# Kernel optimization log

Hardware: AMD Instinct MI355X
Metric: run time of the kernel (lower is better)

Reference implementation:

```python
import jax, jax.numpy as jnp
import numpy as np

NEG = -9e15
LN_EPS = 1e-5
ALPHA = 0.2  # LeakyReLU negative slope


def setup_inputs() -> dict:
    key = jax.random.key(0)
    ks = jax.random.split(key, 10)
    B, N, Din, H, F, L = 8, 512, 64, 8, 128, 2
    x = jax.random.normal(ks[0], (B, N, Din), dtype=jnp.float32)
    adj = jax.random.randint(ks[1], (B, N, N), 0, 2, dtype=jnp.int32)
    Wp = jax.random.normal(ks[2], (Din, F), dtype=jnp.float32) * 0.12
    bp = jnp.zeros((F,), dtype=jnp.float32)
    W_heads = jax.random.normal(ks[3], (L, H, F, F), dtype=jnp.float32) * 0.08
    a_heads = jax.random.normal(ks[4], (L, H, 2 * F), dtype=jnp.float32) * 0.08
    W_out = jax.random.normal(ks[5], (L, H * F, F), dtype=jnp.float32) * 0.03
    a_out = jax.random.normal(ks[6], (L, 2 * F), dtype=jnp.float32) * 0.08
    ln_g = jnp.ones((L, F), dtype=jnp.float32)
    ln_b = jnp.zeros((L, F), dtype=jnp.float32)
    return {"x": x, "adj": adj, "Wp": Wp, "bp": bp, "W_heads": W_heads,
            "a_heads": a_heads, "W_out": W_out, "a_out": a_out,
            "ln_g": ln_g, "ln_b": ln_b}


def _gat_heads(x, W, a, adj_mask):
    # x:[B,N,Fin]  W:[H,Fin,F]  a:[H,2F]  adj_mask:[B,N,N] bool
    h = jnp.einsum('bni,hio->bhno', x, W)          # [B,H,N,F]
    F = h.shape[-1]
    # a_input @ a == (h_i . a1) + (h_j . a2): split attention vector,
    # mathematically identical to the concat formulation.
    s1 = jnp.einsum('bhnf,hf->bhn', h, a[:, :F])   # source term
    s2 = jnp.einsum('bhnf,hf->bhn', h, a[:, F:])   # target term
    e = jax.nn.leaky_relu(s1[:, :, :, None] + s2[:, :, None, :], ALPHA)  # [B,H,N,N]
    att = jnp.where(adj_mask[:, None], e, NEG)
    att = jax.nn.softmax(att, axis=-1)
    return jnp.einsum('bhnm,bhmf->bhnf', att, h)   # [B,H,N,F]


def _gat_single(x, W, a, adj_mask):
    # out_att head (concat=False, no ELU)
    h = jnp.einsum('bni,io->bno', x, W)            # [B,N,F]
    F = h.shape[-1]
    s1 = h @ a[:F]                                  # [B,N]
    s2 = h @ a[F:]
    e = jax.nn.leaky_relu(s1[:, :, None] + s2[:, None, :], ALPHA)
    att = jnp.where(adj_mask, e, NEG)
    att = jax.nn.softmax(att, axis=-1)
    return jnp.einsum('bnm,bmf->bnf', att, h)


def _layernorm(x, g, b):
    mu = jnp.mean(x, axis=-1, keepdims=True)
    var = jnp.var(x, axis=-1, keepdims=True)
    return (x - mu) * jax.lax.rsqrt(var + LN_EPS) * g + b


def reference(x, adj, Wp, bp, W_heads, a_heads, W_out, a_out, ln_g, ln_b):
    adj_mask = adj > 0                              # [B,N,N]
    L = W_heads.shape[0]
    B, N = x.shape[0], x.shape[1]
    # input projection (eval mode -> dropout is identity)
    h = jax.nn.relu(x @ Wp + bp)                    # [B,N,F]
    for i in range(L):
        residual = h
        heads = _gat_heads(h, W_heads[i], a_heads[i], adj_mask)      # [B,H,N,F]
        heads = jax.nn.elu(heads)                                     # concat=True -> ELU
        multi = jnp.transpose(heads, (0, 2, 1, 3)).reshape(B, N, -1)  # [B,N,H*F]
        out = _gat_single(multi, W_out[i], a_out[i], adj_mask)        # [B,N,F]
        h = _layernorm(out + residual, ln_g[i], ln_b[i])
        if i < L - 1:
            h = jax.nn.relu(h)
    return h
```

## Files before the change

### kernel.cpp

```cpp
#include <hip/hip_runtime.h>


constexpr int B = 8, N = 512, DIN = 64, H = 8, F = 128;
constexpr int BN = B * N;
constexpr float ALPHA_LR = 0.2f;
constexpr float EPS_LN = 1e-5f;
constexpr float FLOW = -3.0e38f;

typedef __attribute__((ext_vector_type(8))) short short8;
typedef __attribute__((ext_vector_type(4))) float f32x4;

__device__ __forceinline__ f32x4 mfma16(short8 a, short8 b, f32x4 c) {
  return __builtin_amdgcn_mfma_f32_16x16x32_bf16(a, b, c, 0, 0, 0);
}

__device__ __forceinline__ short f2bf(float f) {
  union { float f; unsigned u; } v;
  v.f = f;
  unsigned r = v.u + 0x7FFFu + ((v.u >> 16) & 1u);
  return (short)(r >> 16);
}

__global__ __launch_bounds__(256) void g_setup(
    const float* __restrict__ x, const int* __restrict__ adj,
    const float* __restrict__ Wp, const float* __restrict__ bp,
    const float* __restrict__ W_heads, const float* __restrict__ W_out,
    float* __restrict__ h, short* __restrict__ hb,
    unsigned long long* __restrict__ amask, short* __restrict__ WTh,
    short* __restrict__ WoT, float* __restrict__ sA) {
  __shared__ float T[32][33];
  __shared__ float xr[2][64];
  int bid = blockIdx.x, tid = threadIdx.x;
  for (int i = tid; i < 288; i += 256) sA[(size_t)bid * 288 + i] = 0.f;
  {
    int lane = tid & 63, wv = tid >> 6;
    int v[16];
#pragma unroll
    for (int j = 0; j < 16; j++) {
      int w = (bid + j * 512) * 4 + wv;
      v[j] = adj[(size_t)w * 64 + lane];
    }
#pragma unroll
    for (int j = 0; j < 16; j++) {
      int w = (bid + j * 512) * 4 + wv;
      unsigned long long m = __ballot(v[j] > 0);
      if (lane == 0) amask[w] = m;
    }
  }
  {
    int half = tid >> 7, f = tid & 127;
    int b = bid & 7, v0 = bid >> 3;
    for (int v = v0; v < 256; v += 64) {
      int row = b * 512 + v * 2 + half;
      __syncthreads();
      if (f < 64) xr[half][f] = x[(size_t)row * DIN + f];
      __syncthreads();
      float acc = bp[f];
#pragma unroll
      for (int i = 0; i < DIN; i++)
        acc = fmaf(xr[half][i], Wp[i * F + f], acc);
      acc = fmaxf(acc, 0.f);
      h[(size_t)row * F + f] = acc;
      hb[(size_t)row * F + f] = f2bf(acc);
    }
  }
  {
    const float* in; short* out; int R, C, bx, by, bt;
    if (bid < 256) {
      in = W_heads; out = WTh; R = 128; C = 128;
      bx = bid & 3; by = (bid >> 2) & 3; bt = bid >> 4;
    } else {
      int i = bid - 256;
      in = W_out; out = WoT; R = 1024; C = 128;
      bx = i & 3; by = (i >> 2) & 31; bt = i >> 7;
    }
    int c0 = bx * 32, r0 = by * 32;
    const float* ip = in + (size_t)bt * R * C;
    short* op = out + (size_t)bt * R * C;
    __syncthreads();
    {
      int r = tid >> 3, c4 = (tid & 7) * 4;
      float4 v = *(const float4*)(ip + (size_t)(r0 + r) * C + c0 + c4);
      T[r][c4] = v.x; T[r][c4 + 1] = v.y; T[r][c4 + 2] = v.z; T[r][c4 + 3] = v.w;
    }
    __syncthreads();
    {
      int cr = tid >> 3, q = (tid & 7) * 4;
      short4 o;
      o.x = f2bf(T[q][cr]); o.y = f2bf(T[q + 1][cr]);
      o.z = f2bf(T[q + 2][cr]); o.w = f2bf(T[q + 3][cr]);
      *(short4*)(op + (size_t)(c0 + cr) * R + r0 + q) = o;
    }
  }
}

__global__ __launch_bounds__(256) void k_proj_heads_mfma2(
    const short* __restrict__ WT, const short* __restrict__ hb,
    const float* __restrict__ ah_base, short* __restrict__ hhT,
    float* __restrict__ s1, float* __restrict__ s2) {
  int bid = blockIdx.x;
  int b = bid & 7, hd = (bid >> 3) & 7, ft = (bid >> 6) & 1, nt = bid >> 7;
  int bh = b * 8 + hd;
  int n0 = nt * 64;
  constexpr int LK = 136;
  __shared__ short As[64 * LK];
  __shared__ short Bs[64 * LK];
  int tid = threadIdx.x, lane = tid & 63, w = tid >> 6;
  {
    int r = tid >> 2, q = tid & 3;
    const uint4* g = (const uint4*)(WT + ((size_t)hd * F + ft * 64 + r) * F) + q * 4;
    uint4* lp = (uint4*)(As + r * LK) + q * 4;
    lp[0] = g[0]; lp[1] = g[1]; lp[2] = g[2]; lp[3] = g[3];
  }
  {
    int r = tid >> 2, q = tid & 3;
    const uint4* g = (const uint4*)(hb + ((size_t)(b * N + n0 + r)) * F) + q * 4;
    uint4* lp = (uint4*)(Bs + r * LK) + q * 4;
    lp[0] = g[0]; lp[1] = g[1]; lp[2] = g[2]; lp[3] = g[3];
  }
  __syncthreads();
  int arow = lane & 15, koff = (lane >> 4) * 8;
  f32x4 acc[4] = {};
#pragma unroll
  for (int ks = 0; ks < 4; ks++) {
    short8 bb = *(const short8*)(Bs + (w * 16 + arow) * LK + ks * 32 + koff);
#pragma unroll
    for (int rt = 0; rt < 4; rt++) {
      short8 a = *(const short8*)(As + (rt * 16 + arow) * LK + ks * 32 + koff);
      acc[rt] = mfma16(a, bb, acc[rt]);
    }
  }
  short* outp = hhT + (size_t)bh * F * N;
  int crow0 = (lane >> 4) * 4;
#pragma unroll
  for (int rt = 0; rt < 4; rt++) {
    int fo = ft * 64 + rt * 16 + crow0;
    int n = n0 + w * 16 + arow;
#pragma unroll
    for (int r = 0; r < 4; r++)
      outp[(size_t)(fo + r) * N + n] = f2bf(acc[rt][r]);
  }
  const float* ah = ah_base + (size_t)hd * 2 * F;
  float pa1 = 0.f, pa2 = 0.f;
#pragma unroll
  for (int rt = 0; rt < 4; rt++) {
    int fo = ft * 64 + rt * 16 + crow0;
#pragma unroll
    for (int r = 0; r < 4; r++) {
      pa1 = fmaf(ah[fo + r], acc[rt][r], pa1);
      pa2 = fmaf(ah[F + fo + r], acc[rt][r], pa2);
    }
  }
  pa1 += __shfl_xor(pa1, 16); pa1 += __shfl_xor(pa1, 32);
  pa2 += __shfl_xor(pa2, 16); pa2 += __shfl_xor(pa2, 32);
  if (lane < 16) {
    int n = n0 + w * 16 + lane;
    atomicAdd(&s1[(size_t)bh * N + n], pa1);
    atomicAdd(&s2[(size_t)bh * N + n], pa2);
  }
}

__global__ __launch_bounds__(256) void k_attn_heads4(
    const short* __restrict__ VT, const float* __restrict__ s1g,
    const float* __restrict__ s2g, const unsigned long long* __restrict__ amask,
    short* __restrict__ multi) {
  int bid = blockIdx.x;
  int b = bid & 7, hd = (bid >> 3) & 7, nt = bid >> 6;
  int bh = b * 8 + hd;
  int n0 = nt * 32;
  constexpr int LVK = 72;
  __shared__ short Vs[128 * LVK];
  __shared__ short Pf[4 * 64 * 8];
  __shared__ float s2all[512];
  __shared__ float s1r[32], mrow[32], linv[32];
  __shared__ float red[32][8];

  int tid = threadIdx.x, lane = tid & 63, w = tid >> 6;
  s2all[tid] = s2g[(size_t)bh * N + tid];
  s2all[tid + 256] = s2g[(size_t)bh * N + tid + 256];
  if (tid < 32) s1r[tid] = s1g[(size_t)bh * N + n0 + tid];
  __syncthreads();
  {
    int r = tid & 31, seg = tid >> 5;
    unsigned long long mb = amask[((size_t)(b * N + n0 + r)) * 8 + seg];
    unsigned lo = (unsigned)mb, hi = (unsigned)(mb >> 32);
    int base = seg * 64;
    float mx = FLOW;
#pragma unroll
    for (int k = 0; k < 32; k++) {
      mx = ((lo >> k) & 1u) ? fmaxf(mx, s2all[base + k]) : mx;
      mx = ((hi >> k) & 1u) ? fmaxf(mx, s2all[base + 32 + k]) : mx;
    }
    red[r][seg] = mx;
  }
  __syncthreads();
  if (tid < 32) {
    float m2 = FLOW;
#pragma unroll
    for (int k = 0; k < 8; k++) m2 = fmaxf(m2, red[tid][k]);
    float xm = s1r[tid] + m2;
    mrow[tid] = xm > 0.f ? xm : ALPHA_LR * xm;
  }
  int prow = ((w >> 1) << 4) | (lane & 15);
  int pcol = ((w & 1) << 5) + ((lane >> 4) << 3);
  int pg = ((w & 1) << 2) | (lane >> 4);
  const unsigned long long* mp = amask + ((size_t)(b * N + n0 + prow)) * 8;
  float lp = 0.f;
  int arow = lane & 15, koff = (lane >> 4) * 8;
  f32x4 acc[2][2] = {};
  const short* Vg = VT + (size_t)bh * F * N;
  int fr = tid >> 1, hf = tid & 1;
  for (int mc = 0; mc < 8; mc++) {
    int m0 = mc * 64;
    __syncthreads();
    {
      const uint4* g4 = (const uint4*)(Vg + (size_t)fr * N + m0 + hf * 32);
      uint4* l4 = (uint4*)(Vs + fr * LVK + hf * 32);
      l4[0] = g4[0]; l4[1] = g4[1]; l4[2] = g4[2]; l4[3] = g4[3];
    }
    {
      float s1v = s1r[prow], mr = mrow[prow];
      unsigned bits = (unsigned)((mp[mc] >> pcol) & 0xffull);
      short8 pk;
#pragma unroll
      for (int j = 0; j < 8; j++) {
        float xv = s1v + s2all[m0 + pcol + j];
        xv = xv > 0.f ? xv : ALPHA_LR * xv;
        float p = __expf(xv - mr);
        p = ((bits >> j) & 1u) ? p : 0.f;
        lp += p;
        pk[j] = f2bf(p);
      }
      *(short8*)(Pf + (w * 64 + lane) * 8) = pk;
    }
    __syncthreads();
#pragma unroll
    for (int ks = 0; ks < 2; ks++) {
      short8 a0 = *(const short8*)(Pf + ((0 * 2 + ks) * 64 + lane) * 8);
      short8 a1 = *(const short8*)(Pf + ((1 * 2 + ks) * 64 + lane) * 8);
#pragma unroll
      for (int cj = 0; cj < 2; cj++) {
        short8 bb = *(const short8*)(Vs + ((w * 2 + cj) * 16 + arow) * LVK +
                                     ks * 32 + koff);
        acc[0][cj] = mfma16(a0, bb, acc[0][cj]);
        acc[1][cj] = mfma16(a1, bb, acc[1][cj]);
      }
    }
  }
  __syncthreads();
  red[prow][pg] = lp;
  __syncthreads();
  if (tid < 32) {
    float ls = 0.f;
#pragma unroll
    for (int k = 0; k < 8; k++) ls += red[tid][k];
    linv[tid] = 1.f / ls;
  }
  __syncthreads();
  int crow0 = (lane >> 4) * 4;
#pragma unroll
  for (int rt = 0; rt < 2; rt++)
#pragma unroll
    for (int cj = 0; cj < 2; cj++) {
      int fcol = (w * 2 + cj) * 16 + arow;
#pragma unroll
      for (int rr = 0; rr < 4; rr++) {
        int nrow = rt * 16 + crow0 + rr;
        float v = acc[rt][cj][rr] * linv[nrow];
        v = v > 0.f ? v : __expf(v) - 1.f;
        multi[((size_t)(b * N + n0 + nrow)) * (H * F) + hd * F + fcol] = f2bf(v);
      }
    }
}

__global__ __launch_bounds__(256) void k_proj_out_mfma(
    const short* __restrict__ WoT, const short* __restrict__ multi,
    const float* __restrict__ ao, short* __restrict__ hsT,
    float* __restrict__ s1, float* __restrict__ s2) {
  int bid = blockIdx.x;
  int b = bid & 7, ft = (bid >> 3) & 3, nt = bid >> 5;
  constexpr int LK = 136;
  __shared__ short As[32 * LK];
  __shared__ short Bs[64 * LK];
  int tid = threadIdx.x, lane = tid & 63, w = tid >> 6;
  int arow = lane & 15, koff = (lane >> 4) * 8;
  const int KT = H * F;
  f32x4 acc[2] = {};
  for (int k0 = 0; k0 < KT; k0 += 128) {
    __syncthreads();
    {
      int r = tid >> 3, e = tid & 7;
      const uint4* gp = (const uint4*)(WoT + (size_t)(ft * 32 + r) * KT + k0) + e * 2;
      uint4* lp = (uint4*)(As + r * LK) + e * 2;
      lp[0] = gp[0]; lp[1] = gp[1];
    }
    {
      int r = tid >> 2, q = tid & 3;
      const uint4* gp =
          (const uint4*)(multi + (size_t)(b * N + nt * 64 + r) * KT + k0) + q * 4;
      uint4* lp = (uint4*)(Bs + r * LK) + q * 4;
      lp[0] = gp[0]; lp[1] = gp[1]; lp[2] = gp[2]; lp[3] = gp[3];
    }
    __syncthreads();
#pragma unroll
    for (int ks = 0; ks < 4; ks++) {
      short8 b0 = *(const short8*)(Bs + (w * 16 + arow) * LK + ks * 32 + koff);
      short8 a0 = *(const short8*)(As + arow * LK + ks * 32 + koff);
      short8 a1 = *(const short8*)(As + (16 + arow) * LK + ks * 32 + koff);
      acc[0] = mfma16(a0, b0, acc[0]);
      acc[1] = mfma16(a1, b0, acc[1]);
    }
  }
  int crow0 = (lane >> 4) * 4;
  short* op = hsT + (size_t)b * F * N;
#pragma unroll
  for (int rt = 0; rt < 2; rt++)
#pragma unroll
    for (int r = 0; r < 4; r++)
      op[(size_t)(ft * 32 + rt * 16 + crow0 + r) * N + nt * 64 + w * 16 + arow] =
          f2bf(acc[rt][r]);
  float pa1 = 0.f, pa2 = 0.f;
#pragma unroll
  for (int rt = 0; rt < 2; rt++) {
    int fo = ft * 32 + rt * 16 + crow0;
#pragma unroll
    for (int r = 0; r < 4; r++) {
      pa1 = fmaf(ao[fo + r], acc[rt][r], pa1);
      pa2 = fmaf(ao[F + fo + r], acc[rt][r], pa2);
    }
  }
  pa1 += __shfl_xor(pa1, 16); pa1 += __shfl_xor(pa1, 32);
  pa2 += __shfl_xor(pa2, 16); pa2 += __shfl_xor(pa2, 32);
  if (lane < 16) {
    int n = nt * 64 + w * 16 + lane;
    atomicAdd(&s1[(size_t)b * N + n], pa1);
    atomicAdd(&s2[(size_t)b * N + n], pa2);
  }
}

template <int LAST>
__global__ __launch_bounds__(256) void k_attn_single3(
    const short* __restrict__ VT, const float* __restrict__ s1g,
    const float* __restrict__ s2g, const unsigned long long* __restrict__ amask,
    const float* __restrict__ resid, const float* __restrict__ lng,
    const float* __restrict__ lnb, float* __restrict__ hout,
    short* __restrict__ hbout, float* __restrict__ dout) {
  int bid = blockIdx.x;
  int b = bid & 7, nt = bid >> 3;
  int n0 = nt * 16;
  constexpr int LVK = 136;
  __shared__ short Vs[128 * LVK];
  __shared__ short Pf[4 * 64 * 8];
  __shared__ float s2all[512];
  __shared__ float Ot[16][132];
  __shared__ float redS[16][16], redQ[16][16];
  __shared__ float s1r[16], mrow[16], linv[16], muA[16], rsA[16];

  int tid = threadIdx.x, lane = tid & 63, w = tid >> 6;
  s2all[tid] = s2g[(size_t)b * N + tid];
  s2all[tid + 256] = s2g[(size_t)b * N + tid + 256];
  if (tid < 16) s1r[tid] = s1g[(size_t)b * N + n0 + tid];
  __syncthreads();
  {
    int r = tid & 15, seg = tid >> 4;
    unsigned long long mb = amask[((size_t)(b * N + n0 + r)) * 8 + (seg >> 1)];
    unsigned bits = (unsigned)(mb >> ((seg & 1) * 32));
    float mx = FLOW;
#pragma unroll
    for (int k = 0; k < 32; k++)
      mx = ((bits >> k) & 1u) ? fmaxf(mx, s2all[seg * 32 + k]) : mx;
    redS[r][seg] = mx;
  }
  __syncthreads();
  if (tid < 16) {
    float m2 = FLOW;
#pragma unroll
    for (int k = 0; k < 16; k++) m2 = fmaxf(m2, redS[tid][k]);
    float xm = s1r[tid] + m2;
    mrow[tid] = xm > 0.f ? xm : ALPHA_LR * xm;
  }
  float lp = 0.f;
  int arow = lane & 15, koff = (lane >> 4) * 8;
  int pr = tid & 15, pq = (tid >> 4) & 3;
  f32x4 acc[2] = {};
  const short* Vg = VT + (size_t)b * F * N;
  const unsigned long long* mp = amask + ((size_t)(b * N + n0 + pr)) * 8;
  for (int mc = 0; mc < 4; mc++) {
    int m0 = mc * 128;
    __syncthreads();
    {
      int fr = tid >> 1, hf = tid & 1;
      const uint4* g4 = (const uint4*)(Vg + (size_t)fr * N + m0 + hf * 64);
      uint4* l4 = (uint4*)(Vs + fr * LVK + hf * 64);
#pragma unroll
      for (int k = 0; k < 8; k++) l4[k] = g4[k];
    }
    {
      float s1v = s1r[pr], mr = mrow[pr];
      unsigned bits = (unsigned)(mp[mc * 2 + (w >> 1)] >> ((w & 1) * 32));
      short8 pk;
#pragma unroll
      for (int j = 0; j < 8; j++) {
        float xv = s1v + s2all[m0 + w * 32 + pq * 8 + j];
        xv = xv > 0.f ? xv : ALPHA_LR * xv;
        float p = __expf(xv - mr);
        p = ((bits >> (pq * 8 + j)) & 1u) ? p : 0.f;
        lp += p;
        pk[j] = f2bf(p);
      }
      *(short8*)(Pf + (w * 64 + ((pq << 4) | pr)) * 8) = pk;
    }
    __syncthreads();
#pragma unroll
    for (int ks = 0; ks < 4; ks++) {
      short8 a = *(const short8*)(Pf + (ks * 64 + lane) * 8);
#pragma unroll
      for (int cj = 0; cj < 2; cj++) {
        short8 bb = *(const short8*)(Vs + ((w * 2 + cj) * 16 + arow) * LVK +
                                     ks * 32 + koff);
        acc[cj] = mfma16(a, bb, acc[cj]);
      }
    }
  }
  __syncthreads();
  redS[pr][tid >> 4] = lp;
  __syncthreads();
  if (tid < 16) {
    float l = 0.f;
#pragma unroll
    for (int k = 0; k < 16; k++) l += redS[tid][k];
    linv[tid] = 1.f / l;
  }
  __syncthreads();
  int crow0 = (lane >> 4) * 4;
#pragma unroll
  for (int cj = 0; cj < 2; cj++) {
    int fcol = (w * 2 + cj) * 16 + arow;
#pragma unroll
    for (int rr = 0; rr < 4; rr++) {
      int row = crow0 + rr;
      Ot[row][fcol] = acc[cj][rr] * linv[row];
    }
  }
  __syncthreads();
  int r2 = tid >> 4, f8 = (tid & 15) * 8;
  size_t gbase = ((size_t)(b * N + n0 + r2)) * F + f8;
  float v[8];
  float s = 0.f, sq = 0.f;
#pragma unroll
  for (int j = 0; j < 8; j++) {
    float t = Ot[r2][f8 + j] + resid[gbase + j];
    v[j] = t;
    s += t;
    sq = fmaf(t, t, sq);
  }
  redS[r2][tid & 15] = s;
  redQ[r2][tid & 15] = sq;
  __syncthreads();
  if (tid < 16) {
    float ss = 0.f, qq = 0.f;
#pragma unroll
    for (int k = 0; k < 16; k++) { ss += redS[tid][k]; qq += redQ[tid][k]; }
    float mu = ss * (1.f / F);
    muA[tid] = mu;
    rsA[tid] = rsqrtf(qq * (1.f / F) - mu * mu + EPS_LN);
  }
  __syncthreads();
  float mu = muA[r2], rs = rsA[r2];
#pragma unroll
  for (int j = 0; j < 8; j++) {
    float y = (v[j] - mu) * rs * lng[f8 + j] + lnb[f8 + j];
    if (LAST) {
      dout[gbase + j] = y;
    } else {
      y = fmaxf(y, 0.f);
      hout[gbase + j] = y;
      hbout[gbase + j] = f2bf(y);
    }
  }
}

extern "C" void kernel_launch(void* const* d_in, const int* in_sizes, int n_in,
                              void* d_out, int out_size, void* d_ws,
                              size_t ws_size, hipStream_t stream) {
  const float* x = (const float*)d_in[0];
  const int* adj = (const int*)d_in[1];
  const float* Wp = (const float*)d_in[2];
  const float* bp = (const float*)d_in[3];
  const float* W_heads = (const float*)d_in[4];
  const float* a_heads = (const float*)d_in[5];
  const float* W_out = (const float*)d_in[6];
  const float* a_out = (const float*)d_in[7];
  const float* ln_g = (const float*)d_in[8];
  const float* ln_b = (const float*)d_in[9];

  char* p = (char*)d_ws;
  auto alloc = [&](size_t bytes) {
    char* r = p;
    p += (bytes + 255) & ~(size_t)255;
    return r;
  };
  float* sA = (float*)alloc((size_t)2 * 73728 * 4);
  short* WTh = (short*)alloc((size_t)2 * H * F * F * 2);
  short* WoT = (short*)alloc((size_t)2 * H * F * F * 2);
  unsigned long long* amask = (unsigned long long*)alloc((size_t)BN * 8 * 8);
  float* h = (float*)alloc((size_t)BN * F * 4);
  short* hb = (short*)alloc((size_t)BN * F * 2);
  short* hhT = (short*)alloc((size_t)B * H * F * N * 2);
  short* multi = (short*)alloc((size_t)BN * H * F * 2);
  short* hsT = (short*)alloc((size_t)B * F * N * 2);

  g_setup<<<512, 256, 0, stream>>>(x, adj, Wp, bp, W_heads, W_out, h, hb,
                                   amask, WTh, WoT, sA);
  for (int l = 0; l < 2; l++) {
    float* s1h = sA + (size_t)l * 73728;
    float* s2h = s1h + 32768;
    float* s1o = s2h + 32768;
    float* s2o = s1o + 4096;
    k_proj_heads_mfma2<<<dim3(1024), 256, 0, stream>>>(
        WTh + (size_t)l * H * F * F, hb, a_heads + (size_t)l * H * 2 * F, hhT,
        s1h, s2h);
    k_attn_heads4<<<dim3(1024), 256, 0, stream>>>(hhT, s1h, s2h, amask, multi);
    k_proj_out_mfma<<<dim3(256), 256, 0, stream>>>(
        WoT + (size_t)l * F * H * F, multi, a_out + (size_t)l * 2 * F, hsT, s1o,
        s2o);
    if (l == 0)
      k_attn_single3<0><<<dim3(256), 256, 0, stream>>>(
          hsT, s1o, s2o, amask, h, ln_g, ln_b, h, hb, nullptr);
    else
      k_attn_single3<1><<<dim3(256), 256, 0, stream>>>(
          hsT, s1o, s2o, amask, h, ln_g + F, ln_b + F, nullptr, nullptr,
          (float*)d_out);
  }
}
```

Before: 178.7 us.

## Double-buffer V and P tiles with register prefetch in attention kernels

Both attention kernels now prefetch the next V chunk from global memory into registers while the current chunk is being processed. They also double-buffer the V and P shared-memory tiles, which removes one barrier per iteration. The single-head kernel additionally moves from 128-wide to 64-wide chunks, so only two waves compute probabilities. The intent is to hide global load latency behind the exp/MFMA work, at the cost of more registers and LDS, and of idle waves during the P computation in the single-head kernel.

```diff
diff --git a/kernel.cpp b/kernel.cpp
--- a/kernel.cpp
+++ b/kernel.cpp
@@ -160,7 +160,7 @@
   }
 }
 
-__global__ __launch_bounds__(256) void k_attn_heads4(
+__global__ __launch_bounds__(256) void k_attn_heads5(
     const short* __restrict__ VT, const float* __restrict__ s1g,
     const float* __restrict__ s2g, const unsigned long long* __restrict__ amask,
     short* __restrict__ multi) {
@@ -169,8 +169,8 @@
   int bh = b * 8 + hd;
   int n0 = nt * 32;
   constexpr int LVK = 72;
-  __shared__ short Vs[128 * LVK];
-  __shared__ short Pf[4 * 64 * 8];
+  __shared__ short Vs[2][128 * LVK];
+  __shared__ short Pf[2][4 * 64 * 8];
   __shared__ float s2all[512];
   __shared__ float s1r[32], mrow[32], linv[32];
   __shared__ float red[32][8];
@@ -179,6 +179,13 @@
   s2all[tid] = s2g[(size_t)bh * N + tid];
   s2all[tid + 256] = s2g[(size_t)bh * N + tid + 256];
   if (tid < 32) s1r[tid] = s1g[(size_t)bh * N + n0 + tid];
+  const short* Vg = VT + (size_t)bh * F * N;
+  int fr = tid >> 1, hf = tid & 1;
+  uint4 vr[4];
+  {
+    const uint4* g4 = (const uint4*)(Vg + (size_t)fr * N + hf * 32);
+    vr[0] = g4[0]; vr[1] = g4[1]; vr[2] = g4[2]; vr[3] = g4[3];
+  }
   __syncthreads();
   {
     int r = tid & 31, seg = tid >> 5;
@@ -201,6 +208,7 @@
     float xm = s1r[tid] + m2;
     mrow[tid] = xm > 0.f ? xm : ALPHA_LR * xm;
   }
+  __syncthreads();
   int prow = ((w >> 1) << 4) | (lane & 15);
   int pcol = ((w & 1) << 5) + ((lane >> 4) << 3);
   int pg = ((w & 1) << 2) | (lane >> 4);
@@ -208,19 +216,16 @@
   float lp = 0.f;
   int arow = lane & 15, koff = (lane >> 4) * 8;
   f32x4 acc[2][2] = {};
-  const short* Vg = VT + (size_t)bh * F * N;
-  int fr = tid >> 1, hf = tid & 1;
   for (int mc = 0; mc < 8; mc++) {
-    int m0 = mc * 64;
-    __syncthreads();
-    {
-      const uint4* g4 = (const uint4*)(Vg + (size_t)fr * N + m0 + hf * 32);
-      uint4* l4 = (uint4*)(Vs + fr * LVK + hf * 32);
-      l4[0] = g4[0]; l4[1] = g4[1]; l4[2] = g4[2]; l4[3] = g4[3];
+    int buf = mc & 1;
+    {
+      uint4* l4 = (uint4*)(Vs[buf] + fr * LVK + hf * 32);
+      l4[0] = vr[0]; l4[1] = vr[1]; l4[2] = vr[2]; l4[3] = vr[3];
     }
     {
       float s1v = s1r[prow], mr = mrow[prow];
       unsigned bits = (unsigned)((mp[mc] >> pcol) & 0xffull);
+      int m0 = mc * 64;
       short8 pk;
 #pragma unroll
       for (int j = 0; j < 8; j++) {
@@ -231,16 +236,21 @@
         lp += p;
         pk[j] = f2bf(p);
       }
-      *(short8*)(Pf + (w * 64 + lane) * 8) = pk;
+      *(short8*)(Pf[buf] + (w * 64 + lane) * 8) = pk;
+    }
+    if (mc < 7) {
+      const uint4* g4 =
+          (const uint4*)(Vg + (size_t)fr * N + (mc + 1) * 64 + hf * 32);
+      vr[0] = g4[0]; vr[1] = g4[1]; vr[2] = g4[2]; vr[3] = g4[3];
     }
     __syncthreads();
 #pragma unroll
     for (int ks = 0; ks < 2; ks++) {
-      short8 a0 = *(const short8*)(Pf + ((0 * 2 + ks) * 64 + lane) * 8);
-      short8 a1 = *(const short8*)(Pf + ((1 * 2 + ks) * 64 + lane) * 8);
+      short8 a0 = *(const short8*)(Pf[buf] + ((0 * 2 + ks) * 64 + lane) * 8);
+      short8 a1 = *(const short8*)(Pf[buf] + ((1 * 2 + ks) * 64 + lane) * 8);
 #pragma unroll
       for (int cj = 0; cj < 2; cj++) {
-        short8 bb = *(const short8*)(Vs + ((w * 2 + cj) * 16 + arow) * LVK +
+        short8 bb = *(const short8*)(Vs[buf] + ((w * 2 + cj) * 16 + arow) * LVK +
                                      ks * 32 + koff);
         acc[0][cj] = mfma16(a0, bb, acc[0][cj]);
         acc[1][cj] = mfma16(a1, bb, acc[1][cj]);
@@ -339,7 +349,7 @@
 }
 
 template <int LAST>
-__global__ __launch_bounds__(256) void k_attn_single3(
+__global__ __launch_bounds__(256) void k_attn_single5(
     const short* __restrict__ VT, const float* __restrict__ s1g,
     const float* __restrict__ s2g, const unsigned long long* __restrict__ amask,
     const float* __restrict__ resid, const float* __restrict__ lng,
@@ -348,9 +358,9 @@
   int bid = blockIdx.x;
   int b = bid & 7, nt = bid >> 3;
   int n0 = nt * 16;
-  constexpr int LVK = 136;
-  __shared__ short Vs[128 * LVK];
-  __shared__ short Pf[4 * 64 * 8];
+  constexpr int LVK = 72;
+  __shared__ short Vs[2][128 * LVK];
+  __shared__ short Pf[2][2 * 64 * 8];
   __shared__ float s2all[512];
   __shared__ float Ot[16][132];
   __shared__ float redS[16][16], redQ[16][16];
@@ -360,6 +370,13 @@
   s2all[tid] = s2g[(size_t)b * N + tid];
   s2all[tid + 256] = s2g[(size_t)b * N + tid + 256];
   if (tid < 16) s1r[tid] = s1g[(size_t)b * N + n0 + tid];
+  const short* Vg = VT + (size_t)b * F * N;
+  int fr = tid >> 1, hf = tid & 1;
+  uint4 vr[4];
+  {
+    const uint4* g4 = (const uint4*)(Vg + (size_t)fr * N + hf * 32);
+    vr[0] = g4[0]; vr[1] = g4[1]; vr[2] = g4[2]; vr[3] = g4[3];
+  }
   __syncthreads();
   {
     int r = tid & 15, seg = tid >> 4;
@@ -379,56 +396,59 @@
     float xm = s1r[tid] + m2;
     mrow[tid] = xm > 0.f ? xm : ALPHA_LR * xm;
   }
+  __syncthreads();
+  int prow = lane & 15;
+  int pcol = (w << 5) + ((lane >> 4) << 3);
+  const unsigned long long* mp = amask + ((size_t)(b * N + n0 + prow)) * 8;
   float lp = 0.f;
   int arow = lane & 15, koff = (lane >> 4) * 8;
-  int pr = tid & 15, pq = (tid >> 4) & 3;
   f32x4 acc[2] = {};
-  const short* Vg = VT + (size_t)b * F * N;
-  const unsigned long long* mp = amask + ((size_t)(b * N + n0 + pr)) * 8;
-  for (int mc = 0; mc < 4; mc++) {
-    int m0 = mc * 128;
-    __syncthreads();
-    {
-      int fr = tid >> 1, hf = tid & 1;
-      const uint4* g4 = (const uint4*)(Vg + (size_t)fr * N + m0 + hf * 64);
-      uint4* l4 = (uint4*)(Vs + fr * LVK + hf * 64);
-#pragma unroll
-      for (int k = 0; k < 8; k++) l4[k] = g4[k];
-    }
-    {
-      float s1v = s1r[pr], mr = mrow[pr];
-      unsigned bits = (unsigned)(mp[mc * 2 + (w >> 1)] >> ((w & 1) * 32));
+  for (int mc = 0; mc < 8; mc++) {
+    int buf = mc & 1;
+    {
+      uint4* l4 = (uint4*)(Vs[buf] + fr * LVK + hf * 32);
+      l4[0] = vr[0]; l4[1] = vr[1]; l4[2] = vr[2]; l4[3] = vr[3];
+    }
+    if (w < 2) {
+      float s1v = s1r[prow], mr = mrow[prow];
+      unsigned bits = (unsigned)((mp[mc] >> pcol) & 0xffull);
+      int m0 = mc * 64;
       short8 pk;
 #pragma unroll
       for (int j = 0; j < 8; j++) {
-        float xv = s1v + s2all[m0 + w * 32 + pq * 8 + j];
+        float xv = s1v + s2all[m0 + pcol + j];
         xv = xv > 0.f ? xv : ALPHA_LR * xv;
         float p = __expf(xv - mr);
-        p = ((bits >> (pq * 8 + j)) & 1u) ? p : 0.f;
+        p = ((bits >> j) & 1u) ? p : 0.f;
         lp += p;
         pk[j] = f2bf(p);
       }
-      *(short8*)(Pf + (w * 64 + ((pq << 4) | pr)) * 8) = pk;
+      *(short8*)(Pf[buf] + (w * 64 + lane) * 8) = pk;
+    }
+    if (mc < 7) {
+      const uint4* g4 =
+          (const uint4*)(Vg + (size_t)fr * N + (mc + 1) * 64 + hf * 32);
+      vr[0] = g4[0]; vr[1] = g4[1]; vr[2] = g4[2]; vr[3] = g4[3];
     }
     __syncthreads();
 #pragma unroll
-    for (int ks = 0; ks < 4; ks++) {
-      short8 a = *(const short8*)(Pf + (ks * 64 + lane) * 8);
+    for (int ks = 0; ks < 2; ks++) {
+      short8 a = *(const short8*)(Pf[buf] + (ks * 64 + lane) * 8);
 #pragma unroll
       for (int cj = 0; cj < 2; cj++) {
-        short8 bb = *(const short8*)(Vs + ((w * 2 + cj) * 16 + arow) * LVK +
+        short8 bb = *(const short8*)(Vs[buf] + ((w * 2 + cj) * 16 + arow) * LVK +
                                      ks * 32 + koff);
         acc[cj] = mfma16(a, bb, acc[cj]);
       }
     }
   }
   __syncthreads();
-  redS[pr][tid >> 4] = lp;
+  if (w < 2) redS[prow][(w << 2) | (lane >> 4)] = lp;
   __syncthreads();
   if (tid < 16) {
     float l = 0.f;
 #pragma unroll
-    for (int k = 0; k < 16; k++) l += redS[tid][k];
+    for (int k = 0; k < 8; k++) l += redS[tid][k];
     linv[tid] = 1.f / l;
   }
   __syncthreads();
@@ -520,15 +540,15 @@
     k_proj_heads_mfma2<<<dim3(1024), 256, 0, stream>>>(
         WTh + (size_t)l * H * F * F, hb, a_heads + (size_t)l * H * 2 * F, hhT,
         s1h, s2h);
-    k_attn_heads4<<<dim3(1024), 256, 0, stream>>>(hhT, s1h, s2h, amask, multi);
+    k_attn_heads5<<<dim3(1024), 256, 0, stream>>>(hhT, s1h, s2h, amask, multi);
     k_proj_out_mfma<<<dim3(256), 256, 0, stream>>>(
         WoT + (size_t)l * F * H * F, multi, a_out + (size_t)l * 2 * F, hsT, s1o,
         s2o);
     if (l == 0)
-      k_attn_single3<0><<<dim3(256), 256, 0, stream>>>(
+      k_attn_single5<0><<<dim3(256), 256, 0, stream>>>(
           hsT, s1o, s2o, amask, h, ln_g, ln_b, h, hb, nullptr);
     else
-      k_attn_single3<1><<<dim3(256), 256, 0, stream>>>(
+      k_attn_single5<1><<<dim3(256), 256, 0, stream>>>(
           hsT, s1o, s2o, amask, h, ln_g + F, ln_b + F, nullptr, nullptr,
           (float*)d_out);
   }
```

Result: slower. 236.4 us (+32.3%).
